# Kernel optimization log

Measured on AMD Instinct MI355X. Metric: run time of the kernel, lower is better.

The kernel has to match this reference:

```python
import jax, jax.numpy as jnp
import numpy as np

ATT_SIZE = 32
HEAD_NUM = 2


def setup_inputs() -> dict:
    key = jax.random.key(0)
    k_in, k_q, k_k, k_v, k_r = jax.random.split(key, 5)
    B, F, D = 16384, 32, 64
    H = ATT_SIZE * HEAD_NUM  # 64
    inputs = jax.random.normal(k_in, (B, F, D), dtype=jnp.float32)
    W_Query = jax.random.truncated_normal(k_q, -2.0, 2.0, (D, H), dtype=jnp.float32) * 0.05
    W_Key = jax.random.truncated_normal(k_k, -2.0, 2.0, (D, H), dtype=jnp.float32) * 0.05
    W_Value = jax.random.truncated_normal(k_v, -2.0, 2.0, (D, H), dtype=jnp.float32) * 0.05
    W_Res = jax.random.truncated_normal(k_r, -2.0, 2.0, (D, H), dtype=jnp.float32) * 0.05
    return {"inputs": inputs, "W_Query": W_Query, "W_Key": W_Key, "W_Value": W_Value, "W_Res": W_Res}


def reference(inputs, W_Query, W_Key, W_Value, W_Res):
    B, F, D = inputs.shape
    h, a = HEAD_NUM, ATT_SIZE
    # project and reshape to [B, h, F, a]
    q = jnp.einsum('bfd,de->bfe', inputs, W_Query).reshape(B, F, h, a).transpose(0, 2, 1, 3)
    k = jnp.einsum('bfd,de->bfe', inputs, W_Key).reshape(B, F, h, a).transpose(0, 2, 1, 3)
    v = jnp.einsum('bfd,de->bfe', inputs, W_Value).reshape(B, F, h, a).transpose(0, 2, 1, 3)
    # NOTE: original code has NO 1/sqrt(d) scaling
    scores = jnp.einsum('bhqa,bhka->bhqk', q, k)
    attn = jax.nn.softmax(scores, axis=-1)
    out = jnp.einsum('bhqk,bhka->bhqa', attn, v)  # [B, h, F, a]
    out = out.transpose(0, 2, 1, 3).reshape(B, F, h * a)
    out = out + jnp.einsum('bfd,de->bfe', inputs, W_Res)
    return jax.nn.relu(out)
```

## Files before the change

### kernel.cpp

```cpp
#include <hip/hip_runtime.h>


constexpr int kF = 32, kD = 64, kH = 64;

constexpr int XS = 72;
constexpr int QS = 72;
constexpr int VS = 40;
constexpr int PS = 40;

using short8   = __attribute__((ext_vector_type(8))) short;
using float4v  = __attribute__((ext_vector_type(4))) float;
using ushort4v = __attribute__((ext_vector_type(4))) unsigned short;

__device__ __forceinline__ unsigned short f2bf(float x) {
    return __builtin_bit_cast(unsigned short, (__bf16)x);
}
__device__ __forceinline__ float bf2f(unsigned short b) {
    return __uint_as_float((unsigned)b << 16);
}

__global__ void wprep_kernel(const float* __restrict__ Wq, const float* __restrict__ Wk,
                             const float* __restrict__ Wv, const float* __restrict__ Wr,
                             unsigned short* __restrict__ wt) {
    const int m = blockIdx.x;
    const float* __restrict__ W = (m == 0) ? Wq : (m == 1) ? Wk : (m == 2) ? Wv : Wr;
    for (int i = threadIdx.x; i < kD * kH; i += blockDim.x) {
        const int e = i >> 6, d = i & 63;
        wt[m * kD * kH + e * kD + d] = f2bf(W[d * kH + e]);
    }
}

__global__ __launch_bounds__(256)
void interact_mfma(const float* __restrict__ X, const unsigned short* __restrict__ Wt,
                   float* __restrict__ out)
{
    __shared__ __align__(16) unsigned short s_xp[2 * kF * PS];
    __shared__ __align__(16) unsigned short s_q [kF * QS];
    __shared__ __align__(16) unsigned short s_k [kF * QS];
    __shared__ __align__(16) unsigned short s_vt[kH * VS];

    const int t    = threadIdx.x;
    const int w    = t >> 6;
    const int lane = t & 63;
    const int quad = lane >> 4;
    const int l    = lane & 15;
    const int b    = blockIdx.x;
    const int h    = w >> 1;
    const int wmt  = w & 1;

    short8 bfrag[4][2];
    if (w < 3) {
        const unsigned short* __restrict__ wtm = Wt + w * (kD * kH);
        #pragma unroll
        for (int nt = 0; nt < 4; ++nt)
            #pragma unroll
            for (int ks = 0; ks < 2; ++ks)
                bfrag[nt][ks] =
                    *reinterpret_cast<const short8*>(wtm + (16 * nt + l) * kD + 32 * ks + quad * 8);
    }
    short8 rfrag[2][2];
    {
        const unsigned short* __restrict__ wtr = Wt + 3 * (kD * kH);
        #pragma unroll
        for (int j = 0; j < 2; ++j)
            #pragma unroll
            for (int ks = 0; ks < 2; ++ks)
                rfrag[j][ks] = *reinterpret_cast<const short8*>(
                    wtr + (16 * (2 * h + j) + l) * kD + 32 * ks + quad * 8);
    }

    const float* __restrict__ Xb = X + (size_t)b * (kF * kD);
    #pragma unroll
    for (int i = 0; i < 2; ++i) {
        const int idx = i * 256 + t;
        const int f = idx >> 4, c = idx & 15;
        const float4 v = reinterpret_cast<const float4*>(Xb)[idx];
        ushort4v pk = { f2bf(v.x), f2bf(v.y), f2bf(v.z), f2bf(v.w) };
        *reinterpret_cast<ushort4v*>(&s_xp[f * XS + c * 4]) = pk;
    }
    __syncthreads();

    short8 afrag[2][2];
    #pragma unroll
    for (int mt = 0; mt < 2; ++mt)
        #pragma unroll
        for (int ks = 0; ks < 2; ++ks)
            afrag[mt][ks] =
                *reinterpret_cast<const short8*>(&s_xp[(16 * mt + l) * XS + 32 * ks + quad * 8]);

    float4v accr[2];
    accr[0] = (float4v){0.f, 0.f, 0.f, 0.f};
    accr[1] = (float4v){0.f, 0.f, 0.f, 0.f};
    #pragma unroll
    for (int j = 0; j < 2; ++j)
        #pragma unroll
        for (int ks = 0; ks < 2; ++ks)
            accr[j] = __builtin_amdgcn_mfma_f32_16x16x32_bf16(
                afrag[wmt][ks], rfrag[j][ks], accr[j], 0, 0, 0);

    if (w < 3) {
        float4v acc[2][4];
        #pragma unroll
        for (int mt = 0; mt < 2; ++mt)
            #pragma unroll
            for (int nt = 0; nt < 4; ++nt)
                acc[mt][nt] = (float4v){0.f, 0.f, 0.f, 0.f};

        #pragma unroll
        for (int mt = 0; mt < 2; ++mt)
            #pragma unroll
            for (int nt = 0; nt < 4; ++nt) {
                acc[mt][nt] = __builtin_amdgcn_mfma_f32_16x16x32_bf16(
                    afrag[mt][0], bfrag[nt][0], acc[mt][nt], 0, 0, 0);
                acc[mt][nt] = __builtin_amdgcn_mfma_f32_16x16x32_bf16(
                    afrag[mt][1], bfrag[nt][1], acc[mt][nt], 0, 0, 0);
            }

        if (w == 2) {
            #pragma unroll
            for (int mt = 0; mt < 2; ++mt)
                #pragma unroll
                for (int nt = 0; nt < 4; ++nt) {
                    ushort4v pk = { f2bf(acc[mt][nt][0]), f2bf(acc[mt][nt][1]),
                                    f2bf(acc[mt][nt][2]), f2bf(acc[mt][nt][3]) };
                    *reinterpret_cast<ushort4v*>(
                        &s_vt[(16 * nt + l) * VS + 16 * mt + 4 * quad]) = pk;
                }
        } else {
            unsigned short* __restrict__ dst = (w == 0) ? s_q : s_k;
            #pragma unroll
            for (int mt = 0; mt < 2; ++mt)
                #pragma unroll
                for (int nt = 0; nt < 4; ++nt)
                    #pragma unroll
                    for (int r = 0; r < 4; ++r)
                        dst[(16 * mt + quad * 4 + r) * QS + 16 * nt + l] = f2bf(acc[mt][nt][r]);
        }
    }
    __syncthreads();

    {
        const short8 qa =
            *reinterpret_cast<const short8*>(&s_q[(16 * wmt + l) * QS + 32 * h + quad * 8]);
        const short8 kb0 =
            *reinterpret_cast<const short8*>(&s_k[(l) * QS + 32 * h + quad * 8]);
        const short8 kb1 =
            *reinterpret_cast<const short8*>(&s_k[(16 + l) * QS + 32 * h + quad * 8]);

        float4v s0 = (float4v){0.f, 0.f, 0.f, 0.f};
        float4v s1 = (float4v){0.f, 0.f, 0.f, 0.f};
        s0 = __builtin_amdgcn_mfma_f32_16x16x32_bf16(qa, kb0, s0, 0, 0, 0);
        s1 = __builtin_amdgcn_mfma_f32_16x16x32_bf16(qa, kb1, s1, 0, 0, 0);

        #pragma unroll
        for (int r = 0; r < 4; ++r) {
            const int row = 16 * wmt + quad * 4 + r;
            s_xp[(h * kF + row) * PS + l]      = f2bf(__expf(s0[r]));
            s_xp[(h * kF + row) * PS + 16 + l] = f2bf(__expf(s1[r]));
        }
    }

    {
        const short8 pa =
            *reinterpret_cast<const short8*>(&s_xp[(h * kF + 16 * wmt + l) * PS + quad * 8]);
        const short8 vb0 =
            *reinterpret_cast<const short8*>(&s_vt[(32 * h + l) * VS + quad * 8]);
        const short8 vb1 =
            *reinterpret_cast<const short8*>(&s_vt[(32 * h + 16 + l) * VS + quad * 8]);
        const short8 ones = (short8)(short)0x3F80;

        float4v o0 = (float4v){0.f, 0.f, 0.f, 0.f};
        float4v o1 = (float4v){0.f, 0.f, 0.f, 0.f};
        float4v os = (float4v){0.f, 0.f, 0.f, 0.f};
        o0 = __builtin_amdgcn_mfma_f32_16x16x32_bf16(pa, vb0, o0, 0, 0, 0);
        o1 = __builtin_amdgcn_mfma_f32_16x16x32_bf16(pa, vb1, o1, 0, 0, 0);
        os = __builtin_amdgcn_mfma_f32_16x16x32_bf16(pa, ones, os, 0, 0, 0);

        float* __restrict__ Ob = out + (size_t)b * (kF * kH);
        #pragma unroll
        for (int r = 0; r < 4; ++r) {
            const int f = 16 * wmt + quad * 4 + r;
            const float inv = __builtin_amdgcn_rcpf(os[r]);
            Ob[f * kH + 32 * h + l]      = fmaxf(o0[r] * inv + accr[0][r], 0.0f);
            Ob[f * kH + 32 * h + 16 + l] = fmaxf(o1[r] * inv + accr[1][r], 0.0f);
        }
    }
}

extern "C" void kernel_launch(void* const* d_in, const int* in_sizes, int n_in,
                              void* d_out, int out_size, void* d_ws, size_t ws_size,
                              hipStream_t stream) {
    const float* X  = (const float*)d_in[0];
    const float* Wq = (const float*)d_in[1];
    const float* Wk = (const float*)d_in[2];
    const float* Wv = (const float*)d_in[3];
    const float* Wr = (const float*)d_in[4];
    float* out = (float*)d_out;
    unsigned short* wt = (unsigned short*)d_ws;

    wprep_kernel<<<4, 256, 0, stream>>>(Wq, Wk, Wv, Wr, wt);

    const int B = in_sizes[0] / (kF * kD);
    interact_mfma<<<B, 256, 0, stream>>>(X, wt, out);
}
```

Before: 323.7 us.

## Swizzle LDS layouts and give the residual projection its own wave

Replaces the padded shared-memory row strides with XOR-swizzled unpadded layouts for X, Q, K, V^T and the softmax scratch. The residual projection moves from a small per-wave MFMA into a dedicated fourth wave that writes a transposed R tile to LDS, which the epilogue then reads back. Launch bounds now request 8 blocks per SM. This balances MFMA work across all four waves and aims to cut bank conflicts and register pressure, but the residual now passes through bf16 storage and costs extra LDS traffic.

```diff
diff --git a/kernel.cpp b/kernel.cpp
--- a/kernel.cpp
+++ b/kernel.cpp
@@ -2,11 +2,6 @@
 
 
 constexpr int kF = 32, kD = 64, kH = 64;
-
-constexpr int XS = 72;
-constexpr int QS = 72;
-constexpr int VS = 40;
-constexpr int PS = 40;
 
 using short8   = __attribute__((ext_vector_type(8))) short;
 using float4v  = __attribute__((ext_vector_type(4))) float;
@@ -17,6 +12,12 @@
 }
 __device__ __forceinline__ float bf2f(unsigned short b) {
     return __uint_as_float((unsigned)b << 16);
+}
+__device__ __forceinline__ int sw64(int row, int blk) {
+    return blk ^ ((row ^ (row >> 1)) & 7);
+}
+__device__ __forceinline__ int sw32(int row, int blk) {
+    return blk ^ ((row ^ (row >> 2)) & 3);
 }
 
 __global__ void wprep_kernel(const float* __restrict__ Wq, const float* __restrict__ Wk,
@@ -30,14 +31,15 @@
     }
 }
 
-__global__ __launch_bounds__(256)
+__global__ __launch_bounds__(256, 8)
 void interact_mfma(const float* __restrict__ X, const unsigned short* __restrict__ Wt,
                    float* __restrict__ out)
 {
-    __shared__ __align__(16) unsigned short s_xp[2 * kF * PS];
-    __shared__ __align__(16) unsigned short s_q [kF * QS];
-    __shared__ __align__(16) unsigned short s_k [kF * QS];
-    __shared__ __align__(16) unsigned short s_vt[kH * VS];
+    __shared__ __align__(16) unsigned short s_xp[2048];
+    __shared__ __align__(16) unsigned short s_q [2048];
+    __shared__ __align__(16) unsigned short s_k [2048];
+    __shared__ __align__(16) unsigned short s_vt[2048];
+    __shared__ __align__(16) unsigned short s_rt[2048];
 
     const int t    = threadIdx.x;
     const int w    = t >> 6;
@@ -49,7 +51,7 @@
     const int wmt  = w & 1;
 
     short8 bfrag[4][2];
-    if (w < 3) {
+    {
         const unsigned short* __restrict__ wtm = Wt + w * (kD * kH);
         #pragma unroll
         for (int nt = 0; nt < 4; ++nt)
@@ -57,16 +59,6 @@
             for (int ks = 0; ks < 2; ++ks)
                 bfrag[nt][ks] =
                     *reinterpret_cast<const short8*>(wtm + (16 * nt + l) * kD + 32 * ks + quad * 8);
-    }
-    short8 rfrag[2][2];
-    {
-        const unsigned short* __restrict__ wtr = Wt + 3 * (kD * kH);
-        #pragma unroll
-        for (int j = 0; j < 2; ++j)
-            #pragma unroll
-            for (int ks = 0; ks < 2; ++ks)
-                rfrag[j][ks] = *reinterpret_cast<const short8*>(
-                    wtr + (16 * (2 * h + j) + l) * kD + 32 * ks + quad * 8);
     }
 
     const float* __restrict__ Xb = X + (size_t)b * (kF * kD);
@@ -76,29 +68,22 @@
         const int f = idx >> 4, c = idx & 15;
         const float4 v = reinterpret_cast<const float4*>(Xb)[idx];
         ushort4v pk = { f2bf(v.x), f2bf(v.y), f2bf(v.z), f2bf(v.w) };
-        *reinterpret_cast<ushort4v*>(&s_xp[f * XS + c * 4]) = pk;
+        *reinterpret_cast<ushort4v*>(
+            &s_xp[f * 64 + sw64(f, c >> 1) * 8 + (c & 1) * 4]) = pk;
     }
     __syncthreads();
 
-    short8 afrag[2][2];
-    #pragma unroll
-    for (int mt = 0; mt < 2; ++mt)
-        #pragma unroll
-        for (int ks = 0; ks < 2; ++ks)
-            afrag[mt][ks] =
-                *reinterpret_cast<const short8*>(&s_xp[(16 * mt + l) * XS + 32 * ks + quad * 8]);
-
-    float4v accr[2];
-    accr[0] = (float4v){0.f, 0.f, 0.f, 0.f};
-    accr[1] = (float4v){0.f, 0.f, 0.f, 0.f};
-    #pragma unroll
-    for (int j = 0; j < 2; ++j)
-        #pragma unroll
-        for (int ks = 0; ks < 2; ++ks)
-            accr[j] = __builtin_amdgcn_mfma_f32_16x16x32_bf16(
-                afrag[wmt][ks], rfrag[j][ks], accr[j], 0, 0, 0);
-
-    if (w < 3) {
+    {
+        short8 afrag[2][2];
+        #pragma unroll
+        for (int mt = 0; mt < 2; ++mt)
+            #pragma unroll
+            for (int ks = 0; ks < 2; ++ks) {
+                const int row = 16 * mt + l;
+                afrag[mt][ks] = *reinterpret_cast<const short8*>(
+                    &s_xp[row * 64 + sw64(row, 4 * ks + quad) * 8]);
+            }
+
         float4v acc[2][4];
         #pragma unroll
         for (int mt = 0; mt < 2; ++mt)
@@ -116,36 +101,42 @@
                     afrag[mt][1], bfrag[nt][1], acc[mt][nt], 0, 0, 0);
             }
 
-        if (w == 2) {
-            #pragma unroll
-            for (int mt = 0; mt < 2; ++mt)
-                #pragma unroll
-                for (int nt = 0; nt < 4; ++nt) {
-                    ushort4v pk = { f2bf(acc[mt][nt][0]), f2bf(acc[mt][nt][1]),
-                                    f2bf(acc[mt][nt][2]), f2bf(acc[mt][nt][3]) };
-                    *reinterpret_cast<ushort4v*>(
-                        &s_vt[(16 * nt + l) * VS + 16 * mt + 4 * quad]) = pk;
-                }
-        } else {
+        if (w < 2) {
             unsigned short* __restrict__ dst = (w == 0) ? s_q : s_k;
             #pragma unroll
             for (int mt = 0; mt < 2; ++mt)
                 #pragma unroll
                 for (int nt = 0; nt < 4; ++nt)
                     #pragma unroll
-                    for (int r = 0; r < 4; ++r)
-                        dst[(16 * mt + quad * 4 + r) * QS + 16 * nt + l] = f2bf(acc[mt][nt][r]);
+                    for (int r = 0; r < 4; ++r) {
+                        const int row = 16 * mt + quad * 4 + r;
+                        dst[row * 64 + sw64(row, 2 * nt + (l >> 3)) * 8 + (l & 7)] =
+                            f2bf(acc[mt][nt][r]);
+                    }
+        } else {
+            unsigned short* __restrict__ dstT = (w == 2) ? s_vt : s_rt;
+            #pragma unroll
+            for (int mt = 0; mt < 2; ++mt)
+                #pragma unroll
+                for (int nt = 0; nt < 4; ++nt) {
+                    const int e = 16 * nt + l;
+                    ushort4v pk = { f2bf(acc[mt][nt][0]), f2bf(acc[mt][nt][1]),
+                                    f2bf(acc[mt][nt][2]), f2bf(acc[mt][nt][3]) };
+                    *reinterpret_cast<ushort4v*>(
+                        &dstT[e * 32 + sw32(e, 2 * mt + (quad >> 1)) * 8 + (quad & 1) * 4]) = pk;
+                }
         }
     }
     __syncthreads();
 
     {
-        const short8 qa =
-            *reinterpret_cast<const short8*>(&s_q[(16 * wmt + l) * QS + 32 * h + quad * 8]);
-        const short8 kb0 =
-            *reinterpret_cast<const short8*>(&s_k[(l) * QS + 32 * h + quad * 8]);
-        const short8 kb1 =
-            *reinterpret_cast<const short8*>(&s_k[(16 + l) * QS + 32 * h + quad * 8]);
+        const int qrow = 16 * wmt + l;
+        const short8 qa = *reinterpret_cast<const short8*>(
+            &s_q[qrow * 64 + sw64(qrow, 4 * h + quad) * 8]);
+        const short8 kb0 = *reinterpret_cast<const short8*>(
+            &s_k[l * 64 + sw64(l, 4 * h + quad) * 8]);
+        const short8 kb1 = *reinterpret_cast<const short8*>(
+            &s_k[(16 + l) * 64 + sw64(16 + l, 4 * h + quad) * 8]);
 
         float4v s0 = (float4v){0.f, 0.f, 0.f, 0.f};
         float4v s1 = (float4v){0.f, 0.f, 0.f, 0.f};
@@ -154,19 +145,20 @@
 
         #pragma unroll
         for (int r = 0; r < 4; ++r) {
-            const int row = 16 * wmt + quad * 4 + r;
-            s_xp[(h * kF + row) * PS + l]      = f2bf(__expf(s0[r]));
-            s_xp[(h * kF + row) * PS + 16 + l] = f2bf(__expf(s1[r]));
+            const int rowG = h * kF + 16 * wmt + quad * 4 + r;
+            s_xp[rowG * 32 + sw32(rowG, l >> 3) * 8 + (l & 7)]       = f2bf(__expf(s0[r]));
+            s_xp[rowG * 32 + sw32(rowG, 2 + (l >> 3)) * 8 + (l & 7)] = f2bf(__expf(s1[r]));
         }
     }
 
     {
-        const short8 pa =
-            *reinterpret_cast<const short8*>(&s_xp[(h * kF + 16 * wmt + l) * PS + quad * 8]);
-        const short8 vb0 =
-            *reinterpret_cast<const short8*>(&s_vt[(32 * h + l) * VS + quad * 8]);
-        const short8 vb1 =
-            *reinterpret_cast<const short8*>(&s_vt[(32 * h + 16 + l) * VS + quad * 8]);
+        const int prow = h * kF + 16 * wmt + l;
+        const short8 pa = *reinterpret_cast<const short8*>(
+            &s_xp[prow * 32 + sw32(prow, quad) * 8]);
+        const short8 vb0 = *reinterpret_cast<const short8*>(
+            &s_vt[(32 * h + l) * 32 + sw32(32 * h + l, quad) * 8]);
+        const short8 vb1 = *reinterpret_cast<const short8*>(
+            &s_vt[(32 * h + 16 + l) * 32 + sw32(32 * h + 16 + l, quad) * 8]);
         const short8 ones = (short8)(short)0x3F80;
 
         float4v o0 = (float4v){0.f, 0.f, 0.f, 0.f};
@@ -176,13 +168,18 @@
         o1 = __builtin_amdgcn_mfma_f32_16x16x32_bf16(pa, vb1, o1, 0, 0, 0);
         os = __builtin_amdgcn_mfma_f32_16x16x32_bf16(pa, ones, os, 0, 0, 0);
 
+        const ushort4v rA = *reinterpret_cast<const ushort4v*>(
+            &s_rt[(32 * h + l) * 32 + sw32(32 * h + l, 2 * wmt + (quad >> 1)) * 8 + (quad & 1) * 4]);
+        const ushort4v rB = *reinterpret_cast<const ushort4v*>(
+            &s_rt[(32 * h + 16 + l) * 32 + sw32(32 * h + 16 + l, 2 * wmt + (quad >> 1)) * 8 + (quad & 1) * 4]);
+
         float* __restrict__ Ob = out + (size_t)b * (kF * kH);
         #pragma unroll
         for (int r = 0; r < 4; ++r) {
             const int f = 16 * wmt + quad * 4 + r;
             const float inv = __builtin_amdgcn_rcpf(os[r]);
-            Ob[f * kH + 32 * h + l]      = fmaxf(o0[r] * inv + accr[0][r], 0.0f);
-            Ob[f * kH + 32 * h + 16 + l] = fmaxf(o1[r] * inv + accr[1][r], 0.0f);
+            Ob[f * kH + 32 * h + l]      = fmaxf(o0[r] * inv + bf2f(rA[r]), 0.0f);
+            Ob[f * kH + 32 * h + 16 + l] = fmaxf(o1[r] * inv + bf2f(rB[r]), 0.0f);
         }
     }
 }
```

Result: faster. 278.3 us (-14.0%).
